# Kernel tuning notes

Hardware: AMD Instinct MI355X
Metric: run time of the kernel (lower is better)

Reference implementation:

```python
import jax, jax.numpy as jnp
import numpy as np


def _sage_mean_layer(x, src, dst, W_self, W_neigh, b):
    # DGL SAGEConv('mean'): h_neigh = mean_{u in N(v)} x_u ; out = x@W_self + h_neigh@W_neigh + b
    n = x.shape[0]
    msg_sum = jax.ops.segment_sum(x[src], dst, num_segments=n)          # [N, D] scatter-add
    deg = jax.ops.segment_sum(jnp.ones_like(dst, dtype=x.dtype), dst, num_segments=n)
    h_neigh = msg_sum / jnp.maximum(deg, 1.0)[:, None]                   # zero-degree nodes -> 0
    return x @ W_self + h_neigh @ W_neigh + b


def setup_inputs() -> dict:
    key = jax.random.key(0)
    ks = jax.random.split(key, 9)
    N, E, D_in, D_hid, D_out = 50000, 800000, 128, 128, 128
    s = lambda d: 1.0 / np.sqrt(d)
    return {
        "x": jax.random.normal(ks[0], (N, D_in), dtype=jnp.float32),
        "src": jax.random.randint(ks[1], (E,), 0, N, dtype=jnp.int32),
        "dst": jax.random.randint(ks[2], (E,), 0, N, dtype=jnp.int32),
        "W1_self": jax.random.uniform(ks[3], (D_in, D_hid), jnp.float32, -s(D_in), s(D_in)),
        "W1_neigh": jax.random.uniform(ks[4], (D_in, D_hid), jnp.float32, -s(D_in), s(D_in)),
        "b1": jnp.zeros((D_hid,), jnp.float32),
        "W2_self": jax.random.uniform(ks[5], (D_hid, D_out), jnp.float32, -s(D_hid), s(D_hid)),
        "W2_neigh": jax.random.uniform(ks[6], (D_hid, D_out), jnp.float32, -s(D_hid), s(D_hid)),
        "b2": jnp.zeros((D_out,), jnp.float32),
    }


def reference(x, src, dst, W1_self, W1_neigh, b1, W2_self, W2_neigh, b2):
    # layer 1: SAGEConv -> ELU (dropout is identity in eval mode)
    h = jax.nn.elu(_sage_mean_layer(x, src, dst, W1_self, W1_neigh, b1))
    # layer 2: is_out_layer=True -> no activation
    return _sage_mean_layer(h, src, dst, W2_self, W2_neigh, b2)
```

## Files before the change

### kernel.cpp

```cpp
#include <hip/hip_runtime.h>
#include <hip/hip_bf16.h>
#include <math.h>

#define DD 128
#define CAP 64
#define NSHARD 8

#define FILL_BLOCKS 4096
#define PACK_BLOCKS 256

typedef __attribute__((ext_vector_type(8))) short short8;
typedef __attribute__((ext_vector_type(4))) float floatx4;
typedef __attribute__((ext_vector_type(8))) unsigned short ushortx8;

static __device__ __forceinline__ unsigned pack2bf(float a, float b) {
    __hip_bfloat16 ba = __float2bfloat16(a), bb = __float2bfloat16(b);
    return (unsigned)*(ushort*)&ba | ((unsigned)*(ushort*)&bb << 16);
}

__global__ __launch_bounds__(256) void prep_kernel(
        const float* __restrict__ x,
        const int* __restrict__ src, const int* __restrict__ dst,
        int* __restrict__ cnt, int* __restrict__ slot,
        const float* __restrict__ W1a, const float* __restrict__ W1b,
        const float* __restrict__ W2a, const float* __restrict__ W2b,
        ushort* __restrict__ Wp1, ushort* __restrict__ Wp2,
        ushort* __restrict__ Xb,
        int E, int n8, int shard_size, int cast_blocks) {
    int b = blockIdx.x;
    if (b < FILL_BLOCKS) {
        int shard = b & (NSHARD - 1);
        int chunk = b >> 3;
        int lo = shard * shard_size;
        int hi = lo + shard_size;
        const int stride = (FILL_BLOCKS >> 3) * 256;
        int e = chunk * 256 + threadIdx.x;
        for (; e + 3 * stride < E; e += 4 * stride) {
            int d0 = dst[e];
            int d1 = dst[e + stride];
            int d2 = dst[e + 2 * stride];
            int d3 = dst[e + 3 * stride];
            if (d0 >= lo && d0 < hi) {
                int p = atomicAdd(&cnt[d0], 1);
                if (p < CAP) slot[(size_t)d0 * CAP + p] = src[e];
            }
            if (d1 >= lo && d1 < hi) {
                int p = atomicAdd(&cnt[d1], 1);
                if (p < CAP) slot[(size_t)d1 * CAP + p] = src[e + stride];
            }
            if (d2 >= lo && d2 < hi) {
                int p = atomicAdd(&cnt[d2], 1);
                if (p < CAP) slot[(size_t)d2 * CAP + p] = src[e + 2 * stride];
            }
            if (d3 >= lo && d3 < hi) {
                int p = atomicAdd(&cnt[d3], 1);
                if (p < CAP) slot[(size_t)d3 * CAP + p] = src[e + 3 * stride];
            }
        }
        for (; e < E; e += stride) {
            int d = dst[e];
            if (d >= lo && d < hi) {
                int p = atomicAdd(&cnt[d], 1);
                if (p < CAP) slot[(size_t)d * CAP + p] = src[e];
            }
        }
    } else if (b < FILL_BLOCKS + cast_blocks) {
        int i = (b - FILL_BLOCKS) * 256 + threadIdx.x;
        if (i < n8) {
            const float4* xp = (const float4*)x;
            float4 v0 = xp[(size_t)i * 2];
            float4 v1 = xp[(size_t)i * 2 + 1];
            uint4 o;
            o.x = pack2bf(v0.x, v0.y);
            o.y = pack2bf(v0.z, v0.w);
            o.z = pack2bf(v1.x, v1.y);
            o.w = pack2bf(v1.z, v1.w);
            *(uint4*)&Xb[(size_t)i * 8] = o;
        }
    } else {
        int gid = (b - FILL_BLOCKS - cast_blocks) * 256 + threadIdx.x;
        int layer = gid >> 15;
        int r = gid & 32767;
        int j = r & 7;
        int lane = (r >> 3) & 63;
        int nt = (r >> 9) & 7;
        int ks = r >> 12;
        int k = ks * 32 + (lane >> 4) * 8 + j;
        int col = nt * 16 + (lane & 15);
        const float* W = layer ? (k < 128 ? W2a : W2b) : (k < 128 ? W1a : W1b);
        float v = W[(k & 127) * DD + col];
        __hip_bfloat16 bf = __float2bfloat16(v);
        (layer ? Wp2 : Wp1)[r] = *(ushort*)&bf;
    }
}

#define BF2F(u) __uint_as_float((unsigned)(u) << 16)

__global__ __launch_bounds__(256) void agg_mean_kernel(
        const ushort* __restrict__ Xb, const int* __restrict__ cnt,
        const int* __restrict__ slot, ushort* __restrict__ Hn, int n) {
    int v = (blockIdx.x * blockDim.x + threadIdx.x) >> 6;
    int lane = threadIdx.x & 63;
    if (v >= n) return;
    int d = cnt[v];
    if (d > CAP) d = CAP;
    int g = lane >> 4;
    int sl = lane & 15;
    int c = sl * 8;

    float acc[8];
#pragma unroll
    for (int j = 0; j < 8; ++j) acc[j] = 0.f;

    if (d > 0) {
        int li = lane < d ? lane : d - 1;
        int idx = slot[(size_t)v * CAP + li];
        int i = 0;
        for (; i + 16 <= d; i += 16) {
            int u0 = __shfl(idx, i + 0 + g);
            int u1 = __shfl(idx, i + 4 + g);
            int u2 = __shfl(idx, i + 8 + g);
            int u3 = __shfl(idx, i + 12 + g);
            ushortx8 y0 = *(const ushortx8*)&Xb[(size_t)u0 * DD + c];
            ushortx8 y1 = *(const ushortx8*)&Xb[(size_t)u1 * DD + c];
            ushortx8 y2 = *(const ushortx8*)&Xb[(size_t)u2 * DD + c];
            ushortx8 y3 = *(const ushortx8*)&Xb[(size_t)u3 * DD + c];
#pragma unroll
            for (int j = 0; j < 8; ++j)
                acc[j] += BF2F((ushort)y0[j]) + BF2F((ushort)y1[j])
                        + BF2F((ushort)y2[j]) + BF2F((ushort)y3[j]);
        }
        for (; i < d; i += 4) {
            int srcl = i + g;
            int valid = srcl < d;
            int u = __shfl(idx, valid ? srcl : (d - 1));
            float w = valid ? 1.f : 0.f;
            ushortx8 y = *(const ushortx8*)&Xb[(size_t)u * DD + c];
#pragma unroll
            for (int j = 0; j < 8; ++j) acc[j] += w * BF2F((ushort)y[j]);
        }
    }

#pragma unroll
    for (int j = 0; j < 8; ++j) {
        acc[j] += __shfl_xor(acc[j], 16);
        acc[j] += __shfl_xor(acc[j], 32);
    }

    if (g == 0) {
        float inv = 1.0f / (float)(d > 0 ? d : 1);
        ushort tmp[8];
#pragma unroll
        for (int j = 0; j < 8; ++j) {
            __hip_bfloat16 b = __float2bfloat16(acc[j] * inv);
            tmp[j] = *(ushort*)&b;
        }
        uint4 ov;
        ov.x = (unsigned)tmp[0] | ((unsigned)tmp[1] << 16);
        ov.y = (unsigned)tmp[2] | ((unsigned)tmp[3] << 16);
        ov.z = (unsigned)tmp[4] | ((unsigned)tmp[5] << 16);
        ov.w = (unsigned)tmp[6] | ((unsigned)tmp[7] << 16);
        *(uint4*)&Hn[(size_t)v * DD + c] = ov;
    }
}

__global__ __launch_bounds__(256) void gemm_fused_kernel(
        const ushort* __restrict__ Xb, const ushort* __restrict__ Hn,
        const ushort* __restrict__ Wp, const float* __restrict__ bias,
        ushort* __restrict__ out_bf16, float* __restrict__ out_f32,
        int nstrips, int do_elu) {
    int strip = blockIdx.x * 4 + (threadIdx.x >> 6);
    if (strip >= nstrips) return;
    int lane = threadIdx.x & 63;
    int m = lane & 15;
    int quad = lane >> 4;
    const size_t row0 = (size_t)strip * 16;
    const ushort* xrow = Xb + (row0 + m) * DD + quad * 8;
    const ushort* hrow = Hn + (row0 + m) * DD + quad * 8;

    floatx4 acc[8];
#pragma unroll
    for (int t = 0; t < 8; ++t) acc[t] = (floatx4){0.f, 0.f, 0.f, 0.f};

#pragma unroll
    for (int ks = 0; ks < 8; ++ks) {
        short8 a = (ks < 4) ? *(const short8*)(xrow + ks * 32)
                            : *(const short8*)(hrow + (ks - 4) * 32);
        const ushort* wp = Wp + ((size_t)(ks * 8) * 64 + lane) * 8;
#pragma unroll
        for (int nt = 0; nt < 8; ++nt) {
            short8 b = *(const short8*)(wp + (size_t)nt * 64 * 8);
            acc[nt] = __builtin_amdgcn_mfma_f32_16x16x32_bf16(a, b, acc[nt], 0, 0, 0);
        }
    }

#pragma unroll
    for (int nt = 0; nt < 8; ++nt) {
        int col = nt * 16 + m;
        float bv = bias[col];
#pragma unroll
        for (int r = 0; r < 4; ++r) {
            size_t row = row0 + quad * 4 + r;
            float v = acc[nt][r] + bv;
            if (do_elu) v = v > 0.f ? v : expm1f(v);
            if (out_f32) {
                out_f32[row * DD + col] = v;
            } else {
                __hip_bfloat16 b = __float2bfloat16(v);
                out_bf16[row * DD + col] = *(ushort*)&b;
            }
        }
    }
}


extern "C" void kernel_launch(void* const* d_in, const int* in_sizes, int n_in,
                              void* d_out, int out_size, void* d_ws, size_t ws_size,
                              hipStream_t stream) {
    const float* x   = (const float*)d_in[0];
    const int*   src = (const int*)d_in[1];
    const int*   dst = (const int*)d_in[2];
    const float* W1s = (const float*)d_in[3];
    const float* W1n = (const float*)d_in[4];
    const float* b1  = (const float*)d_in[5];
    const float* W2s = (const float*)d_in[6];
    const float* W2n = (const float*)d_in[7];
    const float* b2  = (const float*)d_in[8];
    float* out = (float*)d_out;

    const int N = in_sizes[0] / DD;
    const int E = in_sizes[1];

    char* ws = (char*)d_ws;
    int* cnt       = (int*)ws; ws += (size_t)N * 4;
    int* slot      = (int*)ws; ws += (size_t)N * CAP * 4;
    ushort* Wp1    = (ushort*)ws; ws += 65536;
    ushort* Wp2    = (ushort*)ws; ws += 65536;
    ushort* Xb     = (ushort*)ws; ws += (size_t)N * DD * 2;
    ushort* Hn     = (ushort*)ws; ws += (size_t)N * DD * 2;
    ushort* H1     = (ushort*)ws; ws += (size_t)N * DD * 2;

    (void)hipMemsetAsync(cnt, 0, (size_t)N * 4, stream);

    const int shard_size = (N + NSHARD - 1) / NSHARD;
    const int n8 = N * DD / 8;
    const int cast_blocks = (n8 + 255) / 256;
    prep_kernel<<<FILL_BLOCKS + cast_blocks + PACK_BLOCKS, 256, 0, stream>>>(
        x, src, dst, cnt, slot, W1s, W1n, W2s, W2n, Wp1, Wp2, Xb,
        E, n8, shard_size, cast_blocks);

    const int nstrips = N / 16;
    const int gb = (nstrips + 3) / 4;
    const int ab = (N * 64 + 255) / 256;

    agg_mean_kernel<<<ab, 256, 0, stream>>>(Xb, cnt, slot, Hn, N);
    gemm_fused_kernel<<<gb, 256, 0, stream>>>(Xb, Hn, Wp1, b1, H1, nullptr, nstrips, 1);

    agg_mean_kernel<<<ab, 256, 0, stream>>>(H1, cnt, slot, Hn, N);
    gemm_fused_kernel<<<gb, 256, 0, stream>>>(H1, Hn, Wp2, b2, nullptr, out, nstrips, 0);
}
```

Baseline: 235.1 us.

## Fuse neighbor aggregation into GEMM via LDS and simplify edge fill

Merges the mean-aggregation kernel and the MFMA GEMM into one per-layer kernel. Each block aggregates 16 rows into shared memory, then the four waves each compute two column tiles of the output. This removes the Hn round trip through global memory and two launches. It also replaces the sharded, unrolled adjacency fill with a simple one-edge-per-thread atomic fill. That may cost some atomic locality and changes slot ordering, and each block now does less GEMM work per wave.

```diff
diff --git a/kernel.cpp b/kernel.cpp
--- a/kernel.cpp
+++ b/kernel.cpp
@@ -4,10 +4,7 @@
 
 #define DD 128
 #define CAP 64
-#define NSHARD 8
-
-#define FILL_BLOCKS 4096
-#define PACK_BLOCKS 256
+#define LDSP 136
 
 typedef __attribute__((ext_vector_type(8))) short short8;
 typedef __attribute__((ext_vector_type(4))) float floatx4;
@@ -17,6 +14,8 @@
     __hip_bfloat16 ba = __float2bfloat16(a), bb = __float2bfloat16(b);
     return (unsigned)*(ushort*)&ba | ((unsigned)*(ushort*)&bb << 16);
 }
+
+#define BF2F(u) __uint_as_float((unsigned)(u) << 16)
 
 __global__ __launch_bounds__(256) void prep_kernel(
         const float* __restrict__ x,
@@ -26,46 +25,18 @@
         const float* __restrict__ W2a, const float* __restrict__ W2b,
         ushort* __restrict__ Wp1, ushort* __restrict__ Wp2,
         ushort* __restrict__ Xb,
-        int E, int n8, int shard_size, int cast_blocks) {
+        int E, int n8, int fill_blocks, int cast_blocks) {
     int b = blockIdx.x;
-    if (b < FILL_BLOCKS) {
-        int shard = b & (NSHARD - 1);
-        int chunk = b >> 3;
-        int lo = shard * shard_size;
-        int hi = lo + shard_size;
-        const int stride = (FILL_BLOCKS >> 3) * 256;
-        int e = chunk * 256 + threadIdx.x;
-        for (; e + 3 * stride < E; e += 4 * stride) {
-            int d0 = dst[e];
-            int d1 = dst[e + stride];
-            int d2 = dst[e + 2 * stride];
-            int d3 = dst[e + 3 * stride];
-            if (d0 >= lo && d0 < hi) {
-                int p = atomicAdd(&cnt[d0], 1);
-                if (p < CAP) slot[(size_t)d0 * CAP + p] = src[e];
-            }
-            if (d1 >= lo && d1 < hi) {
-                int p = atomicAdd(&cnt[d1], 1);
-                if (p < CAP) slot[(size_t)d1 * CAP + p] = src[e + stride];
-            }
-            if (d2 >= lo && d2 < hi) {
-                int p = atomicAdd(&cnt[d2], 1);
-                if (p < CAP) slot[(size_t)d2 * CAP + p] = src[e + 2 * stride];
-            }
-            if (d3 >= lo && d3 < hi) {
-                int p = atomicAdd(&cnt[d3], 1);
-                if (p < CAP) slot[(size_t)d3 * CAP + p] = src[e + 3 * stride];
-            }
-        }
-        for (; e < E; e += stride) {
+    if (b < fill_blocks) {
+        int e = b * 256 + threadIdx.x;
+        if (e < E) {
             int d = dst[e];
-            if (d >= lo && d < hi) {
-                int p = atomicAdd(&cnt[d], 1);
-                if (p < CAP) slot[(size_t)d * CAP + p] = src[e];
-            }
-        }
-    } else if (b < FILL_BLOCKS + cast_blocks) {
-        int i = (b - FILL_BLOCKS) * 256 + threadIdx.x;
+            int s = src[e];
+            int p = atomicAdd(&cnt[d], 1);
+            if (p < CAP) slot[(size_t)d * CAP + p] = s;
+        }
+    } else if (b < fill_blocks + cast_blocks) {
+        int i = (b - fill_blocks) * 256 + threadIdx.x;
         if (i < n8) {
             const float4* xp = (const float4*)x;
             float4 v0 = xp[(size_t)i * 2];
@@ -78,7 +49,7 @@
             *(uint4*)&Xb[(size_t)i * 8] = o;
         }
     } else {
-        int gid = (b - FILL_BLOCKS - cast_blocks) * 256 + threadIdx.x;
+        int gid = (b - fill_blocks - cast_blocks) * 256 + threadIdx.x;
         int layer = gid >> 15;
         int r = gid & 32767;
         int j = r & 7;
@@ -94,120 +65,133 @@
     }
 }
 
-#define BF2F(u) __uint_as_float((unsigned)(u) << 16)
-
-__global__ __launch_bounds__(256) void agg_mean_kernel(
-        const ushort* __restrict__ Xb, const int* __restrict__ cnt,
-        const int* __restrict__ slot, ushort* __restrict__ Hn, int n) {
-    int v = (blockIdx.x * blockDim.x + threadIdx.x) >> 6;
-    int lane = threadIdx.x & 63;
-    if (v >= n) return;
-    int d = cnt[v];
-    if (d > CAP) d = CAP;
-    int g = lane >> 4;
-    int sl = lane & 15;
-    int c = sl * 8;
-
-    float acc[8];
-#pragma unroll
-    for (int j = 0; j < 8; ++j) acc[j] = 0.f;
-
-    if (d > 0) {
-        int li = lane < d ? lane : d - 1;
-        int idx = slot[(size_t)v * CAP + li];
-        int i = 0;
-        for (; i + 16 <= d; i += 16) {
-            int u0 = __shfl(idx, i + 0 + g);
-            int u1 = __shfl(idx, i + 4 + g);
-            int u2 = __shfl(idx, i + 8 + g);
-            int u3 = __shfl(idx, i + 12 + g);
-            ushortx8 y0 = *(const ushortx8*)&Xb[(size_t)u0 * DD + c];
-            ushortx8 y1 = *(const ushortx8*)&Xb[(size_t)u1 * DD + c];
-            ushortx8 y2 = *(const ushortx8*)&Xb[(size_t)u2 * DD + c];
-            ushortx8 y3 = *(const ushortx8*)&Xb[(size_t)u3 * DD + c];
-#pragma unroll
-            for (int j = 0; j < 8; ++j)
-                acc[j] += BF2F((ushort)y0[j]) + BF2F((ushort)y1[j])
-                        + BF2F((ushort)y2[j]) + BF2F((ushort)y3[j]);
-        }
-        for (; i < d; i += 4) {
-            int srcl = i + g;
-            int valid = srcl < d;
-            int u = __shfl(idx, valid ? srcl : (d - 1));
-            float w = valid ? 1.f : 0.f;
-            ushortx8 y = *(const ushortx8*)&Xb[(size_t)u * DD + c];
-#pragma unroll
-            for (int j = 0; j < 8; ++j) acc[j] += w * BF2F((ushort)y[j]);
-        }
-    }
-
-#pragma unroll
-    for (int j = 0; j < 8; ++j) {
-        acc[j] += __shfl_xor(acc[j], 16);
-        acc[j] += __shfl_xor(acc[j], 32);
-    }
-
-    if (g == 0) {
-        float inv = 1.0f / (float)(d > 0 ? d : 1);
-        ushort tmp[8];
+__global__ __launch_bounds__(256) void sage_layer_kernel(
+        const ushort* __restrict__ Xin, const int* __restrict__ cnt,
+        const int* __restrict__ slot, const ushort* __restrict__ Wp,
+        const float* __restrict__ bias,
+        ushort* __restrict__ out_bf16, float* __restrict__ out_f32,
+        int n, int do_elu) {
+    __shared__ ushort hn[16 * LDSP];
+
+    const int row0 = blockIdx.x * 16;
+    const int w    = threadIdx.x >> 6;
+    const int lane = threadIdx.x & 63;
+    const int g  = lane >> 4;
+    const int sl = lane & 15;
+    const int c  = sl * 8;
+
+    int dv[4], idxv[4];
+#pragma unroll
+    for (int t = 0; t < 4; ++t) {
+        int v = row0 + w * 4 + t;
+        dv[t] = (v < n) ? cnt[v] : 0;
+    }
+#pragma unroll
+    for (int t = 0; t < 4; ++t) {
+        int d = dv[t] > CAP ? CAP : dv[t];
+        dv[t] = d;
+        int v = row0 + w * 4 + t;
+        int li = lane < d ? lane : (d - 1);
+        idxv[t] = (d > 0) ? slot[(size_t)v * CAP + li] : 0;
+    }
+
+#pragma unroll
+    for (int t = 0; t < 4; ++t) {
+        const int d = dv[t];
+        const int idx = idxv[t];
+        float acc[8];
+#pragma unroll
+        for (int j = 0; j < 8; ++j) acc[j] = 0.f;
+
+        if (d > 0) {
+            int i = 0;
+            for (; i + 16 <= d; i += 16) {
+                int u0 = __shfl(idx, i + 0 + g);
+                int u1 = __shfl(idx, i + 4 + g);
+                int u2 = __shfl(idx, i + 8 + g);
+                int u3 = __shfl(idx, i + 12 + g);
+                ushortx8 y0 = *(const ushortx8*)&Xin[(size_t)u0 * DD + c];
+                ushortx8 y1 = *(const ushortx8*)&Xin[(size_t)u1 * DD + c];
+                ushortx8 y2 = *(const ushortx8*)&Xin[(size_t)u2 * DD + c];
+                ushortx8 y3 = *(const ushortx8*)&Xin[(size_t)u3 * DD + c];
+#pragma unroll
+                for (int j = 0; j < 8; ++j)
+                    acc[j] += BF2F((ushort)y0[j]) + BF2F((ushort)y1[j])
+                            + BF2F((ushort)y2[j]) + BF2F((ushort)y3[j]);
+            }
+            for (; i < d; i += 4) {
+                int srcl = i + g;
+                int valid = srcl < d;
+                int u = __shfl(idx, valid ? srcl : (d - 1));
+                float wgt = valid ? 1.f : 0.f;
+                ushortx8 y = *(const ushortx8*)&Xin[(size_t)u * DD + c];
+#pragma unroll
+                for (int j = 0; j < 8; ++j) acc[j] += wgt * BF2F((ushort)y[j]);
+            }
+        }
+
 #pragma unroll
         for (int j = 0; j < 8; ++j) {
-            __hip_bfloat16 b = __float2bfloat16(acc[j] * inv);
-            tmp[j] = *(ushort*)&b;
-        }
-        uint4 ov;
-        ov.x = (unsigned)tmp[0] | ((unsigned)tmp[1] << 16);
-        ov.y = (unsigned)tmp[2] | ((unsigned)tmp[3] << 16);
-        ov.z = (unsigned)tmp[4] | ((unsigned)tmp[5] << 16);
-        ov.w = (unsigned)tmp[6] | ((unsigned)tmp[7] << 16);
-        *(uint4*)&Hn[(size_t)v * DD + c] = ov;
-    }
-}
-
-__global__ __launch_bounds__(256) void gemm_fused_kernel(
-        const ushort* __restrict__ Xb, const ushort* __restrict__ Hn,
-        const ushort* __restrict__ Wp, const float* __restrict__ bias,
-        ushort* __restrict__ out_bf16, float* __restrict__ out_f32,
-        int nstrips, int do_elu) {
-    int strip = blockIdx.x * 4 + (threadIdx.x >> 6);
-    if (strip >= nstrips) return;
-    int lane = threadIdx.x & 63;
-    int m = lane & 15;
-    int quad = lane >> 4;
-    const size_t row0 = (size_t)strip * 16;
-    const ushort* xrow = Xb + (row0 + m) * DD + quad * 8;
-    const ushort* hrow = Hn + (row0 + m) * DD + quad * 8;
-
-    floatx4 acc[8];
-#pragma unroll
-    for (int t = 0; t < 8; ++t) acc[t] = (floatx4){0.f, 0.f, 0.f, 0.f};
+            acc[j] += __shfl_xor(acc[j], 16);
+            acc[j] += __shfl_xor(acc[j], 32);
+        }
+
+        if (g == 0) {
+            float inv = 1.0f / (float)(d > 0 ? d : 1);
+            ushort tmp[8];
+#pragma unroll
+            for (int j = 0; j < 8; ++j) {
+                __hip_bfloat16 bq = __float2bfloat16(acc[j] * inv);
+                tmp[j] = *(ushort*)&bq;
+            }
+            uint4 ov;
+            ov.x = (unsigned)tmp[0] | ((unsigned)tmp[1] << 16);
+            ov.y = (unsigned)tmp[2] | ((unsigned)tmp[3] << 16);
+            ov.z = (unsigned)tmp[4] | ((unsigned)tmp[5] << 16);
+            ov.w = (unsigned)tmp[6] | ((unsigned)tmp[7] << 16);
+            *(uint4*)&hn[(w * 4 + t) * LDSP + c] = ov;
+        }
+    }
+
+    __syncthreads();
+
+    const int m = lane & 15;
+    const int quad = lane >> 4;
+    int mrow = row0 + m; if (mrow >= n) mrow = n - 1;
+    const ushort* xrow = Xin + (size_t)mrow * DD + quad * 8;
+    const ushort* hrow = &hn[m * LDSP + quad * 8];
+
+    floatx4 acc0 = (floatx4){0.f, 0.f, 0.f, 0.f};
+    floatx4 acc1 = (floatx4){0.f, 0.f, 0.f, 0.f};
 
 #pragma unroll
     for (int ks = 0; ks < 8; ++ks) {
         short8 a = (ks < 4) ? *(const short8*)(xrow + ks * 32)
                             : *(const short8*)(hrow + (ks - 4) * 32);
         const ushort* wp = Wp + ((size_t)(ks * 8) * 64 + lane) * 8;
-#pragma unroll
-        for (int nt = 0; nt < 8; ++nt) {
-            short8 b = *(const short8*)(wp + (size_t)nt * 64 * 8);
-            acc[nt] = __builtin_amdgcn_mfma_f32_16x16x32_bf16(a, b, acc[nt], 0, 0, 0);
-        }
-    }
-
-#pragma unroll
-    for (int nt = 0; nt < 8; ++nt) {
+        short8 b0 = *(const short8*)(wp + (size_t)(w * 2 + 0) * 64 * 8);
+        short8 b1 = *(const short8*)(wp + (size_t)(w * 2 + 1) * 64 * 8);
+        acc0 = __builtin_amdgcn_mfma_f32_16x16x32_bf16(a, b0, acc0, 0, 0, 0);
+        acc1 = __builtin_amdgcn_mfma_f32_16x16x32_bf16(a, b1, acc1, 0, 0, 0);
+    }
+
+#pragma unroll
+    for (int q = 0; q < 2; ++q) {
+        int nt = w * 2 + q;
         int col = nt * 16 + m;
         float bv = bias[col];
+        floatx4 av = q ? acc1 : acc0;
 #pragma unroll
         for (int r = 0; r < 4; ++r) {
-            size_t row = row0 + quad * 4 + r;
-            float v = acc[nt][r] + bv;
-            if (do_elu) v = v > 0.f ? v : expm1f(v);
+            int row = row0 + quad * 4 + r;
+            if (row >= n) continue;
+            float vv = av[r] + bv;
+            if (do_elu) vv = vv > 0.f ? vv : expm1f(vv);
             if (out_f32) {
-                out_f32[row * DD + col] = v;
+                out_f32[(size_t)row * DD + col] = vv;
             } else {
-                __hip_bfloat16 b = __float2bfloat16(v);
-                out_bf16[row * DD + col] = *(ushort*)&b;
+                __hip_bfloat16 bq = __float2bfloat16(vv);
+                out_bf16[(size_t)row * DD + col] = *(ushort*)&bq;
             }
         }
     }
@@ -237,25 +221,19 @@
     ushort* Wp1    = (ushort*)ws; ws += 65536;
     ushort* Wp2    = (ushort*)ws; ws += 65536;
     ushort* Xb     = (ushort*)ws; ws += (size_t)N * DD * 2;
-    ushort* Hn     = (ushort*)ws; ws += (size_t)N * DD * 2;
     ushort* H1     = (ushort*)ws; ws += (size_t)N * DD * 2;
 
     (void)hipMemsetAsync(cnt, 0, (size_t)N * 4, stream);
 
-    const int shard_size = (N + NSHARD - 1) / NSHARD;
+    const int fill_blocks = (E + 255) / 256;
     const int n8 = N * DD / 8;
     const int cast_blocks = (n8 + 255) / 256;
-    prep_kernel<<<FILL_BLOCKS + cast_blocks + PACK_BLOCKS, 256, 0, stream>>>(
+    prep_kernel<<<fill_blocks + cast_blocks + 256, 256, 0, stream>>>(
         x, src, dst, cnt, slot, W1s, W1n, W2s, W2n, Wp1, Wp2, Xb,
-        E, n8, shard_size, cast_blocks);
-
-    const int nstrips = N / 16;
-    const int gb = (nstrips + 3) / 4;
-    const int ab = (N * 64 + 255) / 256;
-
-    agg_mean_kernel<<<ab, 256, 0, stream>>>(Xb, cnt, slot, Hn, N);
-    gemm_fused_kernel<<<gb, 256, 0, stream>>>(Xb, Hn, Wp1, b1, H1, nullptr, nstrips, 1);
-
-    agg_mean_kernel<<<ab, 256, 0, stream>>>(H1, cnt, slot, Hn, N);
-    gemm_fused_kernel<<<gb, 256, 0, stream>>>(H1, Hn, Wp2, b2, nullptr, out, nstrips, 0);
-}
+        E, n8, fill_blocks, cast_blocks);
+
+    const int nstrips = (N + 15) / 16;
+
+    sage_layer_kernel<<<nstrips, 256, 0, stream>>>(Xb, cnt, slot, Wp1, b1, H1, nullptr, N, 1);
+    sage_layer_kernel<<<nstrips, 256, 0, stream>>>(H1, cnt, slot, Wp2, b2, nullptr, out, N, 0);
+}
```

Result: slower. 243.9 us (+3.8%).
